# Optimization experiments

Measured on AMD Instinct MI355X. Metric: run time of the kernel, lower is better.

Reference implementation:

```python
import jax, jax.numpy as jnp
import numpy as np

EPS = 1e-5
GROUPS1 = 4  # sub_path selects from groups1_list=[4]
GROUPS2 = 1  # sub_path selects from groups2_list=[1]


def _binact(x):
    # ReActNet binary activation: forward = sign(x), backward = piecewise-poly STE
    poly = jnp.where(x < -1.0, -1.0,
           jnp.where(x < 0.0, 2.0 * x + x * x,
           jnp.where(x < 1.0, 2.0 * x - x * x, 1.0)))
    return jax.lax.stop_gradient(jnp.sign(x) - poly) + poly


def _binweight(w):
    # per-output-channel scaled sign with clipped-identity STE
    alpha = jax.lax.stop_gradient(jnp.mean(jnp.abs(w), axis=(1, 2, 3), keepdims=True))
    bw_ng = alpha * jnp.sign(w)
    clip = jnp.clip(w, -1.0, 1.0)
    return jax.lax.stop_gradient(bw_ng - clip) + clip


def _conv(x, w, groups):
    pad = w.shape[-1] // 2  # 'same' padding, stride=1, dilation=1
    return jax.lax.conv_general_dilated(
        x, w, (1, 1), [(pad, pad), (pad, pad)],
        feature_group_count=groups,
        dimension_numbers=('NCHW', 'OIHW', 'NCHW'))


def _bn(x, gamma, beta):
    mu = jnp.mean(x, axis=(0, 2, 3), keepdims=True)
    var = jnp.var(x, axis=(0, 2, 3), keepdims=True)
    return gamma[None, :, None, None] * (x - mu) * jax.lax.rsqrt(var + EPS) + beta[None, :, None, None]


def _bias(x, b):
    return x + b[None, :, None, None]


def _prelu(x, a):
    return jnp.where(x >= 0, x, a[None, :, None, None] * x)


def setup_inputs() -> dict:
    key = jax.random.key(0)
    ks = jax.random.split(key, 4)
    B, C, H = 8, 64, 128
    x = jax.random.normal(ks[0], (B, C, H, H), dtype=jnp.float32)
    w1 = jax.random.normal(ks[1], (C, C // GROUPS1, 3, 3), dtype=jnp.float32) * 0.1
    w2 = jax.random.normal(ks[2], (C, C // GROUPS2, 1, 1), dtype=jnp.float32) * 0.1
    zeros = jnp.zeros((C,), jnp.float32)
    ones = jnp.ones((C,), jnp.float32)
    return {
        'x': x,
        'loss': jnp.zeros((1,), jnp.float32),
        'sub_path': 0,
        'w1': w1, 'w2': w2,
        'bn1_gamma': ones, 'bn1_beta': zeros,
        'bn2_gamma': ones, 'bn2_beta': zeros,
        'b11': zeros, 'b12': zeros, 'b13': zeros,
        'b21': zeros, 'b22': zeros, 'b23': zeros,
        'p1': 0.25 * ones, 'p2': 0.25 * ones,
    }


def reference(x, loss, sub_path, w1, w2, bn1_gamma, bn1_beta, bn2_gamma, bn2_beta,
              b11, b12, b13, b21, b22, b23, p1, p2):
    # branch 1: move -> binact -> 3x3 binary grouped conv -> BN -> residual
    out1 = _binact(_bias(x, b11))
    out1 = _conv(out1, _binweight(w1), GROUPS1)
    out1 = _bn(out1, bn1_gamma, bn1_beta)
    out1 = out1 + x  # adaptive_add: shapes match (stride=1, same channels)
    out1 = _bias(_prelu(_bias(out1, b12), p1), b13)
    # branch 2: move -> binact -> 1x1 binary conv -> BN -> residual
    out2 = _binact(_bias(out1, b21))
    out2 = _conv(out2, _binweight(w2), GROUPS2)
    out2 = _bn(out2, bn2_gamma, bn2_beta)
    out2 = out2 + out1
    out2 = _bias(_prelu(_bias(out2, b22), p2), b23)
    return (out2, loss)
```

## Files before the change

### kernel.cpp

```cpp
#include <hip/hip_runtime.h>
#include <hip/hip_bf16.h>
#include <stdint.h>

typedef unsigned long long ull;

#define B_   8
#define C_   64
#define H_   128
#define W_   128
#define HW_  (H_*W_)
#define NPIX (B_*HW_)
#define NELEM (B_*C_*HW_)
#define G1_  4
#define CPG_ 16
#define TAU_ 5e-5f
#define K2BLKS 512

__global__ __launch_bounds__(256) void k1_conv1(
    const float* __restrict__ x, const float* __restrict__ b11,
    const float* __restrict__ w1,
    int8_t* __restrict__ conv1s, int8_t* __restrict__ conv1sT,
    int* __restrict__ partS1, int* __restrict__ partQ1)
{
    const int orig = blockIdx.y * 64 + blockIdx.x;
    const int swz  = (orig & 7) * 256 + (orig >> 3);
    const int bg = swz >> 6;
    const int tile = swz & 63;
    const int b = bg >> 2, g = bg & 3;
    const int x0 = (tile & 1) * 64;
    const int y0 = (tile >> 1) * 4;

    __shared__ uint32_t sActQ[4][6][66];
    __shared__ uint32_t sAct[6][66];
    __shared__ uint32_t sWpH[2][80], sWnH[2][80];
    __shared__ uint32_t sWp[80], sWn[80];
    __shared__ float cB11[16];
    __shared__ int8_t sS[256][20];
    __shared__ int redS[16][16], redQ[16][16];

    int t = threadIdx.x;
    if (t < 16) cB11[t] = b11[g * CPG_ + t];
    __syncthreads();

    #pragma unroll
    for (int rr = 0; rr < 2; rr++) {
        int id = t + rr * 256;
        if (id < 384) {
            int row = id >> 6, ck = (id & 63) >> 2, q = id & 3;
            int y = y0 - 1 + row;
            uint32_t m0 = 0, m1 = 0, m2 = 0, m3 = 0;
            if (y >= 0 && y < H_) {
                const float* xp = x + ((size_t)b << 20)
                                  + ((size_t)(g * CPG_ + q * 4) << 14)
                                  + y * W_ + x0 + 4 * ck;
                #pragma unroll
                for (int ci = 0; ci < 4; ci++) {
                    int c = q * 4 + ci;
                    float4 v4 = *(const float4*)(xp + ((size_t)ci << 14));
                    float bc = cB11[c];
                    float a0 = __fadd_rn(v4.x, bc), a1 = __fadd_rn(v4.y, bc);
                    float a2 = __fadd_rn(v4.z, bc), a3 = __fadd_rn(v4.w, bc);
                    m0 |= ((a0 > 0.f ? 1u : 0u) << c) | ((a0 != 0.f ? 1u : 0u) << (c + 16));
                    m1 |= ((a1 > 0.f ? 1u : 0u) << c) | ((a1 != 0.f ? 1u : 0u) << (c + 16));
                    m2 |= ((a2 > 0.f ? 1u : 0u) << c) | ((a2 != 0.f ? 1u : 0u) << (c + 16));
                    m3 |= ((a3 > 0.f ? 1u : 0u) << c) | ((a3 != 0.f ? 1u : 0u) << (c + 16));
                }
            }
            sActQ[q][row][4 * ck + 1] = m0;
            sActQ[q][row][4 * ck + 2] = m1;
            sActQ[q][row][4 * ck + 3] = m2;
            sActQ[q][row][4 * ck + 4] = m3;
        } else if (id < 432) {
            int e = id - 384;
            int row = e >> 3, side = (e >> 2) & 1, q = e & 3;
            int y = y0 - 1 + row;
            int xc = side ? (x0 + 64) : (x0 - 1);
            uint32_t m = 0;
            if (y >= 0 && y < H_ && xc >= 0 && xc < W_) {
                const float* xp = x + ((size_t)b << 20)
                                  + ((size_t)(g * CPG_ + q * 4) << 14)
                                  + y * W_ + xc;
                #pragma unroll
                for (int ci = 0; ci < 4; ci++) {
                    int c = q * 4 + ci;
                    float v = __fadd_rn(xp[(size_t)ci << 14], cB11[c]);
                    m |= ((v > 0.f ? 1u : 0u) << c) | ((v != 0.f ? 1u : 0u) << (c + 16));
                }
            }
            sActQ[q][row][side ? 65 : 0] = m;
        }
    }
    if (t < 160) {
        int e = t >> 1, h = t & 1;
        int oc = e / 5, pr = e % 5;
        int o = g * CPG_ + oc;
        int t0 = 2 * pr, t1 = 2 * pr + 1;
        uint32_t p0 = 0, n0 = 0, p1 = 0, n1 = 0;
        for (int i = h * 8; i < h * 8 + 8; i++) {
            float wa = w1[(o * CPG_ + i) * 9 + t0];
            if (wa > 0.f) p0 |= (1u << i);
            if (wa != 0.f) n0 |= (1u << i);
            if (t1 < 9) {
                float wb = w1[(o * CPG_ + i) * 9 + t1];
                if (wb > 0.f) p1 |= (1u << i);
                if (wb != 0.f) n1 |= (1u << i);
            }
        }
        sWpH[h][e] = p0 | (p1 << 16);
        sWnH[h][e] = n0 | (n1 << 16);
    }
    __syncthreads();

    if (t < 80) { sWp[t] = sWpH[0][t] | sWpH[1][t]; sWn[t] = sWnH[0][t] | sWnH[1][t]; }
    {
        int id = t;
        #pragma unroll
        for (int rr = 0; rr < 2; rr++, id += 256) {
            if (id < 396) {
                int row = id / 66, col = id % 66;
                sAct[row][col] = sActQ[0][row][col] | sActQ[1][row][col]
                               | sActQ[2][row][col] | sActQ[3][row][col];
            }
        }
    }
    __syncthreads();

    int tyl = t >> 6, txl = t & 63;
    size_t pixbase = ((size_t)(b * C_ + g * CPG_) << 14)
                   + (size_t)(y0 + tyl) * W_ + x0 + txl;

    uint32_t a[9];
    #pragma unroll
    for (int dy = 0; dy < 3; dy++)
        #pragma unroll
        for (int dx = 0; dx < 3; dx++)
            a[dy * 3 + dx] = sAct[tyl + dy][txl + dx];
    uint32_t ap[5], an[5];
    #pragma unroll
    for (int pr = 0; pr < 4; pr++) {
        ap[pr] = (a[2 * pr] & 0xFFFFu) | (a[2 * pr + 1] << 16);
        an[pr] = (a[2 * pr] >> 16) | (a[2 * pr + 1] & 0xFFFF0000u);
    }
    ap[4] = a[8] & 0xFFFFu;
    an[4] = a[8] >> 16;

    uint32_t tw0 = 0, tw1 = 0, tw2 = 0, tw3 = 0;
    #pragma unroll
    for (int oc = 0; oc < CPG_; oc++) {
        const int wbase = oc * 5;
        int pm = 0, pn = 0;
        #pragma unroll
        for (int pr = 0; pr < 5; pr++) {
            uint32_t nzb = sWn[wbase + pr] & an[pr];
            uint32_t mt  = (~(sWp[wbase + pr] ^ ap[pr])) & nzb;
            pm += __popc(mt);
            pn += __popc(nzb);
        }
        int s = 2 * pm - pn;
        conv1s[pixbase + ((size_t)oc << 14)] = (int8_t)s;
        sS[t][oc] = (int8_t)s;
        uint32_t byte = (uint32_t)(uint8_t)(int8_t)s << ((oc & 3) * 8);
        if ((oc >> 2) == 0) tw0 |= byte;
        else if ((oc >> 2) == 1) tw1 |= byte;
        else if ((oc >> 2) == 2) tw2 |= byte;
        else tw3 |= byte;
    }
    {
        int pix = (b << 14) + (y0 + tyl) * W_ + x0 + txl;
        *(uint4*)(conv1sT + (((size_t)g * NPIX + pix) << 4)) =
            make_uint4(tw0, tw1, tw2, tw3);
    }
    __syncthreads();

    {
        int ch = t & 15, seg = t >> 4;
        int sacc = 0, qacc = 0;
        #pragma unroll
        for (int i = 0; i < 16; i++) {
            int s = (int)sS[seg * 16 + i][ch];
            sacc += s;
            qacc += s * s;
        }
        redS[seg][ch] = sacc; redQ[seg][ch] = qacc;
    }
    __syncthreads();
    if (t < CPG_) {
        int S = 0, Q = 0;
        #pragma unroll
        for (int k = 0; k < 16; k++) { S += redS[k][t]; Q += redQ[k][t]; }
        int bid = bg * 64 + tile;
        partS1[bid * CPG_ + t] = S;
        partQ1[bid * CPG_ + t] = Q;
    }
}

__global__ __launch_bounds__(1024) void f1_bn(
    const float* __restrict__ w1, const float* __restrict__ w2,
    const float* __restrict__ loss, float* __restrict__ loss_out,
    const float* __restrict__ gamma, const float* __restrict__ beta,
    const int* __restrict__ partS1, const int* __restrict__ partQ1,
    float* __restrict__ alpha1f, ull* __restrict__ wpos2, ull* __restrict__ wnz2,
    double* __restrict__ alpha2,
    float* __restrict__ mu_f, float* __restrict__ inv_f,
    float* __restrict__ sA, float* __restrict__ sh)
{
    __shared__ int rS[16][64];
    __shared__ long long rQ[16][64];
    int tid = threadIdx.x;
    int c = tid & 63, j = tid >> 6;
    int g = c >> 4, oc = c & 15;
    int s = 0; long long q = 0;
    for (int i = j; i < 512; i += 16) {
        int bb = i >> 6, bx = i & 63;
        int bid = (bb * 4 + g) * 64 + bx;
        s += partS1[bid * CPG_ + oc];
        q += (long long)partQ1[bid * CPG_ + oc];
    }
    rS[j][c] = s; rQ[j][c] = q;
    __syncthreads();
    if (tid == 0) loss_out[0] = loss[0];
    if (tid < 64) {
        const float* wo = w1 + tid * CPG_ * 9;
        double a = 0.0;
        for (int i = 0; i < CPG_ * 9; i++) a += fabs((double)wo[i]);
        float af = (float)(a / (double)(CPG_ * 9));
        alpha1f[tid] = af;
        double s2 = 0.0; ull pos = 0ull, nzm = 0ull;
        for (int i = 0; i < 64; i++) {
            float w = w2[tid * 64 + i];
            s2 += fabs((double)w);
            if (w > 0.f) pos |= (1ull << i);
            if (w != 0.f) nzm |= (1ull << i);
        }
        alpha2[tid] = s2 / 64.0;
        wpos2[tid] = pos; wnz2[tid] = nzm;
        int S = 0; long long Q = 0;
        #pragma unroll
        for (int k = 0; k < 16; k++) { S += rS[k][tid]; Q += rQ[k][tid]; }
        double n = (double)NPIX;
        double ad = (double)af;
        double sm = (double)S / n;
        double qm = (double)Q / n;
        double mu_d = ad * sm;
        double var_d = ad * ad * (qm - sm * sm);
        double inv_d = 1.0 / sqrt(var_d + 1e-5);
        mu_f[tid] = (float)mu_d;
        inv_f[tid] = (float)inv_d;
        double scale = (double)gamma[tid] * inv_d;
        sA[tid] = (float)(scale * ad);
        sh[tid] = (float)((double)beta[tid] - scale * mu_d);
    }
}

__global__ __launch_bounds__(256) void k2b_pack(
    const int8_t* __restrict__ conv1sT, const float* __restrict__ x,
    const float* __restrict__ alpha1f,
    const float* __restrict__ mu_f, const float* __restrict__ inv_f,
    const float* __restrict__ g1, const float* __restrict__ be1,
    const float* __restrict__ b12, const float* __restrict__ p1, const float* __restrict__ b13,
    const float* __restrict__ b21,
    ulonglong2* __restrict__ packed,
    const ull* __restrict__ wpos2, const ull* __restrict__ wnz2,
    int* __restrict__ partS2, int* __restrict__ partQ2)
{
    __shared__ float cAf[64], cMu[64], cInv[64], cG[64], cB[64],
                     cB12[64], cP1[64], cB13[64], cB21[64];
    __shared__ ull sMaskP[256], sMaskN[256];
    __shared__ int redS[4][64], redQ[4][64];

    int t = threadIdx.x;
    if (t < 64) {
        cAf[t] = alpha1f[t]; cMu[t] = mu_f[t]; cInv[t] = inv_f[t];
        cG[t] = g1[t]; cB[t] = be1[t];
        cB12[t] = b12[t]; cP1[t] = p1[t]; cB13[t] = b13[t]; cB21[t] = b21[t];
    }
    __syncthreads();

    int p = blockIdx.x * 256 + t;
    int b = p >> 14, hw = p & (HW_ - 1);
    const float* xbase = x + ((size_t)b << 20) + hw;
    ull pos = 0ull, nz = 0ull;
    #pragma unroll
    for (int gq = 0; gq < 4; gq++) {
        uint4 rw = *(const uint4*)(conv1sT + (((size_t)gq * NPIX + p) << 4));
        uint32_t wds[4] = {rw.x, rw.y, rw.z, rw.w};
        #pragma unroll
        for (int oc = 0; oc < 16; oc++) {
            const int c = gq * 16 + oc;
            int sv = (int)(wds[oc >> 2] << ((3 - (oc & 3)) * 8)) >> 24;
            float cf = __fmul_rn((float)sv, cAf[c]);
            float v1 = __fsub_rn(cf, cMu[c]);
            float v2 = __fmul_rn(cG[c], v1);
            float v3 = __fmul_rn(v2, cInv[c]);
            float v4 = __fadd_rn(v3, cB[c]);
            float o  = __fadd_rn(v4, xbase[(size_t)c << 14]);
            float tt = __fadd_rn(o, cB12[c]);
            float pr = (tt >= 0.f) ? tt : __fmul_rn(cP1[c], tt);
            float o1 = __fadd_rn(pr, cB13[c]);
            float w  = __fadd_rn(o1, cB21[c]);
            if (w > TAU_)        pos |= (1ull << c);
            if (fabsf(w) > TAU_) nz  |= (1ull << c);
        }
    }
    packed[p] = make_ulonglong2(pos, nz);
    sMaskP[t] = pos; sMaskN[t] = nz;
    __syncthreads();

    int lane = t & 63, wv = t >> 6;
    ull wp = wpos2[lane], wn = wnz2[lane];
    int sacc = 0, qacc = 0;
    const int base = wv * 64;
    #pragma unroll 8
    for (int i = 0; i < 64; i++) {
        ull mp = sMaskP[base + i];
        ull mn = sMaskN[base + i];
        ull nzb = wn & mn;
        ull match = (~(wp ^ mp)) & nzb;
        int s = 2 * __popcll(match) - __popcll(nzb);
        sacc += s;
        qacc += s * s;
    }
    redS[wv][lane] = sacc; redQ[wv][lane] = qacc;
    __syncthreads();
    if (t < 64) {
        partS2[blockIdx.x * 64 + t] = redS[0][t] + redS[1][t] + redS[2][t] + redS[3][t];
        partQ2[blockIdx.x * 64 + t] = redQ[0][t] + redQ[1][t] + redQ[2][t] + redQ[3][t];
    }
}

__global__ __launch_bounds__(1024) void f2_bn(
    const float* __restrict__ gamma, const float* __restrict__ beta,
    const double* __restrict__ alpha,
    const int* __restrict__ partS2, const int* __restrict__ partQ2,
    float* __restrict__ sA, float* __restrict__ sh)
{
    __shared__ int rS[16][64];
    __shared__ long long rQ[16][64];
    int tid = threadIdx.x;
    int c = tid & 63, j = tid >> 6;
    int s = 0; long long q = 0;
    for (int i = j; i < K2BLKS; i += 16) {
        s += partS2[i * 64 + c];
        q += (long long)partQ2[i * 64 + c];
    }
    rS[j][c] = s; rQ[j][c] = q;
    __syncthreads();
    if (tid < 64) {
        int S = 0; long long Q = 0;
        #pragma unroll
        for (int k = 0; k < 16; k++) { S += rS[k][tid]; Q += rQ[k][tid]; }
        double n = (double)NPIX;
        double a = alpha[tid];
        double sm = (double)S / n;
        double qm = (double)Q / n;
        double var = a * a * (qm - sm * sm);
        double inv = 1.0 / sqrt(var + 1e-5);
        double scale = (double)gamma[tid] * inv;
        sA[tid] = (float)(scale * a);
        sh[tid] = (float)((double)beta[tid] - scale * a * sm);
    }
}

__global__ __launch_bounds__(256) void k4_out2(
    const ulonglong2* __restrict__ packed,
    const int8_t* __restrict__ conv1s, const float* __restrict__ x,
    const float* __restrict__ sA1, const float* __restrict__ sh1,
    const float* __restrict__ b12, const float* __restrict__ p1, const float* __restrict__ b13,
    const ull* __restrict__ wpos2, const ull* __restrict__ wnz2,
    const float* __restrict__ sA2, const float* __restrict__ sh2,
    const float* __restrict__ b22, const float* __restrict__ p2, const float* __restrict__ b23,
    float* __restrict__ out2)
{
    int i4 = (blockIdx.x * 256 + threadIdx.x) * 4;
    if (i4 >= NELEM) return;
    int c = (i4 >> 14) & 63;
    int b = i4 >> 20;
    int hw = i4 & (HW_ - 1);
    int p = (b << 14) + hw;
    ull wp = wpos2[c], wn = wnz2[c];
    float a1 = sA1[c], s1c = sh1[c], bb1 = b12[c], pp1 = p1[c], b31 = b13[c];
    float a2 = sA2[c], s2c = sh2[c], bb2 = b22[c], pp2 = p2[c], b32 = b23[c];
    char4 sv = *(const char4*)(conv1s + i4);
    float4 xv = *(const float4*)(x + i4);
    float ss[4] = {(float)sv.x, (float)sv.y, (float)sv.z, (float)sv.w};
    float xx[4] = {xv.x, xv.y, xv.z, xv.w};
    float r[4];
    #pragma unroll
    for (int k = 0; k < 4; k++) {
        float v = a1 * ss[k] + s1c + xx[k];
        float t1 = v + bb1;
        float pr1 = t1 >= 0.f ? t1 : pp1 * t1;
        float o1 = pr1 + b31;
        ulonglong2 pk = packed[p + k];
        ull nzb = wn & pk.y;
        ull match = (~(wp ^ pk.x)) & nzb;
        int s = 2 * __popcll(match) - __popcll(nzb);
        float v2 = a2 * (float)s + s2c + o1;
        float t2 = v2 + bb2;
        float pr2 = t2 >= 0.f ? t2 : pp2 * t2;
        r[k] = pr2 + b32;
    }
    *(float4*)(out2 + i4) = make_float4(r[0], r[1], r[2], r[3]);
}

extern "C" void kernel_launch(void* const* d_in, const int* in_sizes, int n_in,
                              void* d_out, int out_size, void* d_ws, size_t ws_size,
                              hipStream_t stream)
{
    const float* x    = (const float*)d_in[0];
    const float* loss = (const float*)d_in[1];
    const float* w1   = (const float*)d_in[3];
    const float* w2   = (const float*)d_in[4];
    const float* bg1  = (const float*)d_in[5];
    const float* bb1  = (const float*)d_in[6];
    const float* bg2  = (const float*)d_in[7];
    const float* bb2  = (const float*)d_in[8];
    const float* b11  = (const float*)d_in[9];
    const float* b12  = (const float*)d_in[10];
    const float* b13  = (const float*)d_in[11];
    const float* b21  = (const float*)d_in[12];
    const float* b22  = (const float*)d_in[13];
    const float* b23  = (const float*)d_in[14];
    const float* p1   = (const float*)d_in[15];
    const float* p2   = (const float*)d_in[16];
    float* out = (float*)d_out;

    char* ws = (char*)d_ws;
    float* alpha1f   = (float*)(ws + 8192);
    double* alpha2   = (double*)(ws + 12288);
    ull*   wpos2     = (ull*)(ws + 16384);
    ull*   wnz2      = (ull*)(ws + 20480);
    float* mu_f      = (float*)(ws + 24576);
    float* inv_f     = (float*)(ws + 28672);
    float* sA1       = (float*)(ws + 32768);
    float* sh1       = (float*)(ws + 36864);
    float* sA2       = (float*)(ws + 40960);
    float* sh2       = (float*)(ws + 45056);
    int*   partS1    = (int*)(ws + 65536);
    int*   partQ1    = (int*)(ws + 65536 + 131072);
    int*   partS2    = (int*)(ws + 393216);
    int*   partQ2    = (int*)(ws + 393216 + 131072);
    int8_t* conv1s   = (int8_t*)(ws + 1048576);
    ulonglong2* packed = (ulonglong2*)(ws + 1048576 + 8388608);
    int8_t* conv1sT  = (int8_t*)(ws + 1048576 + 8388608 + 2097152);

    k1_conv1<<<dim3(64, 32), 256, 0, stream>>>(x, b11, w1, conv1s, conv1sT,
                                               partS1, partQ1);
    f1_bn<<<1, 1024, 0, stream>>>(w1, w2, loss, out + NELEM, bg1, bb1,
                                  partS1, partQ1, alpha1f, wpos2, wnz2, alpha2,
                                  mu_f, inv_f, sA1, sh1);
    k2b_pack<<<K2BLKS, 256, 0, stream>>>(conv1sT, x, alpha1f, mu_f, inv_f,
                                         bg1, bb1, b12, p1, b13, b21, packed,
                                         wpos2, wnz2, partS2, partQ2);
    f2_bn<<<1, 1024, 0, stream>>>(bg2, bb2, alpha2, partS2, partQ2, sA2, sh2);
    k4_out2<<<NELEM / 1024, 256, 0, stream>>>(packed, conv1s, x, sA1, sh1, b12, p1, b13,
                                              wpos2, wnz2, sA2, sh2, b22, p2, b23, out);
}
```

Measured before the change: 85.90 us.

## Drop NCHW int8 conv1 copy and make final kernel reuse pixel-major conv1 data

k1 no longer writes the channel-major int8 conv1 result and writes only the pixel-major transposed copy. k4 is restructured so each block handles 1024 pixels for one 16-channel group. Each thread loads its packed bits and conv1 vectors once and reuses them across 16 channels, with per-channel constants staged in shared memory. This removes an 8 MB write and read of conv1 and the repeated packed loads per channel. In exchange the grid drops to 512 blocks with more serial work per thread, and x loads and out2 stores are now strided by channel inside the loop.

Measured after the change: 82.03 us, median of 2. 1.05x faster.

```diff
diff --git a/kernel.cpp b/kernel.cpp
--- a/kernel.cpp
+++ b/kernel.cpp
@@ -19,7 +19,7 @@
 __global__ __launch_bounds__(256) void k1_conv1(
     const float* __restrict__ x, const float* __restrict__ b11,
     const float* __restrict__ w1,
-    int8_t* __restrict__ conv1s, int8_t* __restrict__ conv1sT,
+    int8_t* __restrict__ conv1sT,
     int* __restrict__ partS1, int* __restrict__ partQ1)
 {
     const int orig = blockIdx.y * 64 + blockIdx.x;
@@ -126,8 +126,6 @@
     __syncthreads();
 
     int tyl = t >> 6, txl = t & 63;
-    size_t pixbase = ((size_t)(b * C_ + g * CPG_) << 14)
-                   + (size_t)(y0 + tyl) * W_ + x0 + txl;
 
     uint32_t a[9];
     #pragma unroll
@@ -157,7 +155,6 @@
             pn += __popc(nzb);
         }
         int s = 2 * pm - pn;
-        conv1s[pixbase + ((size_t)oc << 14)] = (int8_t)s;
         sS[t][oc] = (int8_t)s;
         uint32_t byte = (uint32_t)(uint8_t)(int8_t)s << ((oc & 3) * 8);
         if ((oc >> 2) == 0) tw0 |= byte;
@@ -363,7 +360,7 @@
 
 __global__ __launch_bounds__(256) void k4_out2(
     const ulonglong2* __restrict__ packed,
-    const int8_t* __restrict__ conv1s, const float* __restrict__ x,
+    const int8_t* __restrict__ conv1sT, const float* __restrict__ x,
     const float* __restrict__ sA1, const float* __restrict__ sh1,
     const float* __restrict__ b12, const float* __restrict__ p1, const float* __restrict__ b13,
     const ull* __restrict__ wpos2, const ull* __restrict__ wnz2,
@@ -371,36 +368,71 @@
     const float* __restrict__ b22, const float* __restrict__ p2, const float* __restrict__ b23,
     float* __restrict__ out2)
 {
-    int i4 = (blockIdx.x * 256 + threadIdx.x) * 4;
-    if (i4 >= NELEM) return;
-    int c = (i4 >> 14) & 63;
-    int b = i4 >> 20;
-    int hw = i4 & (HW_ - 1);
-    int p = (b << 14) + hw;
-    ull wp = wpos2[c], wn = wnz2[c];
-    float a1 = sA1[c], s1c = sh1[c], bb1 = b12[c], pp1 = p1[c], b31 = b13[c];
-    float a2 = sA2[c], s2c = sh2[c], bb2 = b22[c], pp2 = p2[c], b32 = b23[c];
-    char4 sv = *(const char4*)(conv1s + i4);
-    float4 xv = *(const float4*)(x + i4);
-    float ss[4] = {(float)sv.x, (float)sv.y, (float)sv.z, (float)sv.w};
-    float xx[4] = {xv.x, xv.y, xv.z, xv.w};
-    float r[4];
-    #pragma unroll
-    for (int k = 0; k < 4; k++) {
-        float v = a1 * ss[k] + s1c + xx[k];
-        float t1 = v + bb1;
-        float pr1 = t1 >= 0.f ? t1 : pp1 * t1;
-        float o1 = pr1 + b31;
-        ulonglong2 pk = packed[p + k];
-        ull nzb = wn & pk.y;
-        ull match = (~(wp ^ pk.x)) & nzb;
-        int s = 2 * __popcll(match) - __popcll(nzb);
-        float v2 = a2 * (float)s + s2c + o1;
-        float t2 = v2 + bb2;
-        float pr2 = t2 >= 0.f ? t2 : pp2 * t2;
-        r[k] = pr2 + b32;
-    }
-    *(float4*)(out2 + i4) = make_float4(r[0], r[1], r[2], r[3]);
+    const int gq = blockIdx.x & 3;
+    const int pb = blockIdx.x >> 2;
+    const int p0 = pb << 10;
+    const int b = p0 >> 14;
+    const int hw0 = p0 & (HW_ - 1);
+    int t = threadIdx.x;
+
+    __shared__ float cc[10][16];
+    __shared__ ull cwp[16], cwn[16];
+    if (t < 16) {
+        int c = gq * 16 + t;
+        cc[0][t] = sA1[c]; cc[1][t] = sh1[c]; cc[2][t] = b12[c];
+        cc[3][t] = p1[c];  cc[4][t] = b13[c];
+        cc[5][t] = sA2[c]; cc[6][t] = sh2[c]; cc[7][t] = b22[c];
+        cc[8][t] = p2[c];  cc[9][t] = b23[c];
+        cwp[t] = wpos2[c]; cwn[t] = wnz2[c];
+    }
+    __syncthreads();
+
+    const int pq = p0 + 4 * t;
+    ulonglong2 pk0 = packed[pq + 0];
+    ulonglong2 pk1 = packed[pq + 1];
+    ulonglong2 pk2 = packed[pq + 2];
+    ulonglong2 pk3 = packed[pq + 3];
+    uint4 cv0 = *(const uint4*)(conv1sT + (((size_t)gq * NPIX + pq + 0) << 4));
+    uint4 cv1 = *(const uint4*)(conv1sT + (((size_t)gq * NPIX + pq + 1) << 4));
+    uint4 cv2 = *(const uint4*)(conv1sT + (((size_t)gq * NPIX + pq + 2) << 4));
+    uint4 cv3 = *(const uint4*)(conv1sT + (((size_t)gq * NPIX + pq + 3) << 4));
+
+    #pragma unroll
+    for (int oc = 0; oc < 16; oc++) {
+        const int c = gq * 16 + oc;
+        float a1 = cc[0][oc], s1c = cc[1][oc], bb1 = cc[2][oc],
+              pp1 = cc[3][oc], b31 = cc[4][oc];
+        float a2 = cc[5][oc], s2c = cc[6][oc], bb2 = cc[7][oc],
+              pp2 = cc[8][oc], b32 = cc[9][oc];
+        ull wp = cwp[oc], wn = cwn[oc];
+        size_t off = (((size_t)(b * C_ + c)) << 14) + hw0 + 4 * t;
+        float4 xv = *(const float4*)(x + off);
+        float xx[4] = {xv.x, xv.y, xv.z, xv.w};
+        const uint32_t* w0 = (const uint32_t*)&cv0;
+        const uint32_t* w1_ = (const uint32_t*)&cv1;
+        const uint32_t* w2_ = (const uint32_t*)&cv2;
+        const uint32_t* w3_ = (const uint32_t*)&cv3;
+        int sh = (3 - (oc & 3)) * 8, wd = oc >> 2;
+        int sv[4] = { (int)(w0[wd] << sh) >> 24, (int)(w1_[wd] << sh) >> 24,
+                      (int)(w2_[wd] << sh) >> 24, (int)(w3_[wd] << sh) >> 24 };
+        ulonglong2 pks[4] = {pk0, pk1, pk2, pk3};
+        float r[4];
+        #pragma unroll
+        for (int k = 0; k < 4; k++) {
+            float v = a1 * (float)sv[k] + s1c + xx[k];
+            float t1 = v + bb1;
+            float pr1 = t1 >= 0.f ? t1 : pp1 * t1;
+            float o1 = pr1 + b31;
+            ull nzb = wn & pks[k].y;
+            ull match = (~(wp ^ pks[k].x)) & nzb;
+            int s = 2 * __popcll(match) - __popcll(nzb);
+            float v2 = a2 * (float)s + s2c + o1;
+            float t2 = v2 + bb2;
+            float pr2 = t2 >= 0.f ? t2 : pp2 * t2;
+            r[k] = pr2 + b32;
+        }
+        *(float4*)(out2 + off) = make_float4(r[0], r[1], r[2], r[3]);
+    }
 }
 
 extern "C" void kernel_launch(void* const* d_in, const int* in_sizes, int n_in,
@@ -440,12 +472,10 @@
     int*   partQ1    = (int*)(ws + 65536 + 131072);
     int*   partS2    = (int*)(ws + 393216);
     int*   partQ2    = (int*)(ws + 393216 + 131072);
-    int8_t* conv1s   = (int8_t*)(ws + 1048576);
-    ulonglong2* packed = (ulonglong2*)(ws + 1048576 + 8388608);
-    int8_t* conv1sT  = (int8_t*)(ws + 1048576 + 8388608 + 2097152);
-
-    k1_conv1<<<dim3(64, 32), 256, 0, stream>>>(x, b11, w1, conv1s, conv1sT,
-                                               partS1, partQ1);
+    ulonglong2* packed = (ulonglong2*)(ws + 1048576);
+    int8_t* conv1sT  = (int8_t*)(ws + 1048576 + 2097152);
+
+    k1_conv1<<<dim3(64, 32), 256, 0, stream>>>(x, b11, w1, conv1sT, partS1, partQ1);
     f1_bn<<<1, 1024, 0, stream>>>(w1, w2, loss, out + NELEM, bg1, bb1,
                                   partS1, partQ1, alpha1f, wpos2, wnz2, alpha2,
                                   mu_f, inv_f, sA1, sh1);
@@ -453,6 +483,6 @@
                                          bg1, bb1, b12, p1, b13, b21, packed,
                                          wpos2, wnz2, partS2, partQ2);
     f2_bn<<<1, 1024, 0, stream>>>(bg2, bb2, alpha2, partS2, partQ2, sA2, sh2);
-    k4_out2<<<NELEM / 1024, 256, 0, stream>>>(packed, conv1s, x, sA1, sh1, b12, p1, b13,
-                                              wpos2, wnz2, sA2, sh2, b22, p2, b23, out);
-}
+    k4_out2<<<512, 256, 0, stream>>>(packed, conv1sT, x, sA1, sh1, b12, p1, b13,
+                                     wpos2, wnz2, sA2, sh2, b22, p2, b23, out);
+}
```
